# Kernel tuning notes

Measured on AMD Instinct MI355X. Metric: run time of the kernel, lower is better.

## Reference

```python
import jax, jax.numpy as jnp
import numpy as np
from itertools import product

B, C, N = 2, 64, 30000
D, H, W = 64, 64, 64


def _make_shift():
    # itertools.product over (-1,0,1)^3, scaled by 2/(size-1) per axis in (x->W, y->H, z->D) order
    s = np.array(list(product((-1, 0, 1), repeat=3)), dtype=np.float32)  # [27,3]
    scale = np.array([2.0 / (W - 1), 2.0 / (H - 1), 2.0 / (D - 1)], dtype=np.float32)
    return jnp.asarray(s * scale)  # [27,3]


def setup_inputs() -> dict:
    key = jax.random.key(0)
    k1, k2, k3 = jax.random.split(key, 3)
    voxel_features = jax.random.normal(k1, (B, C, D, H, W), dtype=jnp.float32)
    vertices = jax.random.uniform(k2, (B, N, 3), dtype=jnp.float32, minval=-1.0, maxval=1.0)
    # kaiming_normal for relu on a (C, C, 1, 27) conv kernel: std = sqrt(2 / fan_in)
    conv_w = jax.random.normal(k3, (C, C, 27), dtype=jnp.float32) * np.float32(np.sqrt(2.0 / (C * 27)))
    conv_b = jnp.zeros((C,), dtype=jnp.float32)
    return {"voxel_features": voxel_features, "vertices": vertices, "conv_w": conv_w, "conv_b": conv_b}


def _trilinear_sample(vol, grid):
    # vol: [C, D, H, W]; grid: [M, 3] normalized (x, y, z) in [-1, 1]
    # F.grid_sample semantics: mode='bilinear' (trilinear), padding_mode='border', align_corners=True
    sizes_f = jnp.array([W - 1, H - 1, D - 1], dtype=vol.dtype)
    coord = (grid + 1.0) * 0.5 * sizes_f  # unnormalize, align_corners=True
    coord = jnp.clip(coord, 0.0, sizes_f)  # border padding
    c0f = jnp.floor(coord)
    f = coord - c0f  # fractional weights [M,3]
    c0 = c0f.astype(jnp.int32)
    c1 = jnp.minimum(c0 + 1, jnp.array([W - 1, H - 1, D - 1], dtype=jnp.int32))
    x0, y0, z0 = c0[:, 0], c0[:, 1], c0[:, 2]
    x1, y1, z1 = c1[:, 0], c1[:, 1], c1[:, 2]
    fx, fy, fz = f[:, 0], f[:, 1], f[:, 2]

    def g(zi, yi, xi):
        return vol[:, zi, yi, xi]  # [C, M]

    out = (g(z0, y0, x0) * ((1 - fx) * (1 - fy) * (1 - fz))
           + g(z0, y0, x1) * (fx * (1 - fy) * (1 - fz))
           + g(z0, y1, x0) * ((1 - fx) * fy * (1 - fz))
           + g(z0, y1, x1) * (fx * fy * (1 - fz))
           + g(z1, y0, x0) * ((1 - fx) * (1 - fy) * fz)
           + g(z1, y0, x1) * (fx * (1 - fy) * fz)
           + g(z1, y1, x0) * ((1 - fx) * fy * fz)
           + g(z1, y1, x1) * (fx * fy * fz))
    return out  # [C, M]


def reference(voxel_features, vertices, conv_w, conv_b):
    shift = _make_shift()  # [27,3]
    # neighbourhood grid: [B, N, 27, 3] -> flatten to [B, N*27, 3]
    grid = (vertices[:, :, None, :] + shift[None, None, :, :]).reshape(B, N * 27, 3)
    feats = jax.vmap(_trilinear_sample)(voxel_features, grid)  # [B, C, N*27]
    feats = feats.reshape(B, C, N, 27)
    # Conv2d(C, C, kernel=(1,27)) == learned weighted sum over 27 neighbors + channel mix
    out = jnp.einsum("bcnk,ock->bno", feats, conv_w) + conv_b[None, None, :]  # [B, N, C]
    return out
```

## Files before the change

kernel.cpp:

```cpp
#include <hip/hip_runtime.h>
#include <stdint.h>

#define NBATCH 2
#define NVERT  30000
#define VOLCH  16777216ull
#define KDIM   1728
#define ASTR   (KDIM + 8)

typedef __attribute__((ext_vector_type(8))) __bf16 bf16x8;
typedef __attribute__((ext_vector_type(4))) float f32x4;

__device__ __forceinline__ float b2f(unsigned short u) {
  unsigned int x = ((unsigned int)u) << 16;
  return __builtin_bit_cast(float, x);
}

__device__ __forceinline__ unsigned short f2b(float f) {
  unsigned int u = __builtin_bit_cast(unsigned int, f);
  u = (u + 0x7FFFu + ((u >> 16) & 1u)) >> 16;
  return (unsigned short)u;
}

__global__ __launch_bounds__(256) void transpose_vox(
    const float* __restrict__ vox, unsigned short* __restrict__ T) {
  __shared__ float tile[64][65];
  const int b = blockIdx.y;
  const int zy = blockIdx.x;
  const size_t src0 = (size_t)b * 64 * 262144 + (size_t)zy * 64;
#pragma unroll
  for (int i = 0; i < 16; ++i) {
    int idx = i * 256 + threadIdx.x;
    int c = idx >> 6, x = idx & 63;
    tile[c][x] = vox[src0 + (size_t)c * 262144 + x];
  }
  __syncthreads();
  const size_t dst0 = ((size_t)b * 4096 + zy) * 4096;
#pragma unroll
  for (int i = 0; i < 16; ++i) {
    int idx = i * 256 + threadIdx.x;
    int x = idx >> 6, c = idx & 63;
    T[dst0 + x * 64 + c] = f2b(tile[c][x]);
  }
}

__global__ __launch_bounds__(256) void prep_w(
    const float* __restrict__ w, unsigned short* __restrict__ W3) {
  int t = blockIdx.x * 256 + threadIdx.x;
  int o = t / 1728;
  int rem = t - o * 1728;
  int c = rem / 27;
  int k = rem - c * 27;
  int K = k * 64 + c;
  W3[((size_t)(K >> 3) * 64 + o) * 8 + (K & 7)] = f2b(w[t]);
}

__device__ __forceinline__ void axis_setup(float v, int idx[4], float gw[3][4]) {
  float coord = (v + 1.0f) * 0.5f * 63.0f;
  coord = fminf(fmaxf(coord, 0.0f), 63.0f);
  int b0 = (int)coord;
  if (b0 > 63) b0 = 63;
#pragma unroll
  for (int p = 0; p < 4; ++p) {
    int q = b0 - 1 + p;
    idx[p] = min(max(q, 0), 63);
  }
#pragma unroll
  for (int d = 0; d < 3; ++d) {
    float t = coord + (float)(d - 1);
    float tc = fminf(fmaxf(t, 0.0f), 63.0f);
    float fl = floorf(tc);
    int i0 = (int)fl;
    if (i0 > 63) i0 = 63;
    float f = tc - fl;
    int i1 = min(i0 + 1, 63);
    int p0 = i0 - b0 + 1;
    int p1 = i1 - b0 + 1;
#pragma unroll
    for (int p = 0; p < 4; ++p) {
      float g = (p == p0) ? (1.0f - f) : 0.0f;
      g += (p == p1) ? f : 0.0f;
      gw[d][p] = g;
    }
  }
}

__global__ __launch_bounds__(256, 2) void fused_main(
    const float* __restrict__ verts, const unsigned short* __restrict__ T,
    const unsigned short* __restrict__ W3, const float* __restrict__ bias,
    float* __restrict__ out) {
  __shared__ __align__(16) unsigned short A_lds[16][ASTR];
  const int tid = threadIdx.x;
  const int wave = tid >> 6;
  const int lane = tid & 63;
  const int batch = blockIdx.y;
  const int n0 = blockIdx.x * 16;

  const unsigned short* Tb = T + (size_t)batch * VOLCH + lane;

#pragma unroll 1
  for (int vl = 0; vl < 4; ++vl) {
    const int m = wave * 4 + vl;
    const size_t vbase = ((size_t)batch * NVERT + (n0 + m)) * 3;
    const float vx = verts[vbase + 0];
    const float vy = verts[vbase + 1];
    const float vz = verts[vbase + 2];

    int xi[4], yi[4], zi[4];
    float gwx[3][4], gwy[3][4], gwz[3][4];
    axis_setup(vx, xi, gwx);
    axis_setup(vy, yi, gwy);
    axis_setup(vz, zi, gwz);

    int xo[4];
#pragma unroll
    for (int p = 0; p < 4; ++p) xo[p] = xi[p] << 6;

    float fe[3][3][3];
#pragma unroll
    for (int a = 0; a < 3; ++a)
#pragma unroll
      for (int bb = 0; bb < 3; ++bb)
#pragma unroll
        for (int cc = 0; cc < 3; ++cc) fe[a][bb][cc] = 0.0f;

#pragma unroll
    for (int pz = 0; pz < 4; ++pz) {
      float ryv[3][3];
#pragma unroll
      for (int a = 0; a < 3; ++a)
#pragma unroll
        for (int bb = 0; bb < 3; ++bb) ryv[a][bb] = 0.0f;
      const int zoff = zi[pz] << 18;
#pragma unroll
      for (int py = 0; py < 4; ++py) {
        const unsigned short* rp = Tb + zoff + (yi[py] << 12);
        float v0 = b2f(rp[xo[0]]);
        float v1 = b2f(rp[xo[1]]);
        float v2 = b2f(rp[xo[2]]);
        float v3 = b2f(rp[xo[3]]);
        const float wy0 = gwy[0][py], wy1 = gwy[1][py], wy2 = gwy[2][py];
#pragma unroll
        for (int dx = 0; dx < 3; ++dx) {
          float rx = v0 * gwx[dx][0] + v1 * gwx[dx][1] +
                     v2 * gwx[dx][2] + v3 * gwx[dx][3];
          ryv[0][dx] += rx * wy0;
          ryv[1][dx] += rx * wy1;
          ryv[2][dx] += rx * wy2;
        }
      }
#pragma unroll
      for (int dz = 0; dz < 3; ++dz) {
        const float wz = gwz[dz][pz];
#pragma unroll
        for (int dy = 0; dy < 3; ++dy)
#pragma unroll
          for (int dx = 0; dx < 3; ++dx) fe[dz][dy][dx] += ryv[dy][dx] * wz;
      }
    }

    unsigned short* arow = &A_lds[m][0];
#pragma unroll
    for (int dz = 0; dz < 3; ++dz)
#pragma unroll
      for (int dy = 0; dy < 3; ++dy)
#pragma unroll
        for (int dx = 0; dx < 3; ++dx) {
          int k = dx * 9 + dy * 3 + dz;
          arow[(k << 6) + lane] = f2b(fe[dz][dy][dx]);
        }
  }
  __syncthreads();

  const int g = lane >> 4;
  const int r = lane & 15;
  const int o0 = wave * 16;
  f32x4 acc = {0.0f, 0.0f, 0.0f, 0.0f};
  const unsigned short* aptr = &A_lds[r][g * 8];
  const unsigned short* bptr = W3 + (size_t)(g * 64 + o0 + r) * 8;
  for (int kk = 0; kk < 54; ++kk) {
    bf16x8 a = *reinterpret_cast<const bf16x8*>(aptr + kk * 32);
    bf16x8 b = *reinterpret_cast<const bf16x8*>(bptr + (size_t)kk * 2048);
    acc = __builtin_amdgcn_mfma_f32_16x16x32_bf16(a, b, acc, 0, 0, 0);
  }

  const int oc = o0 + r;
  const float bo = bias[oc];
  float* op = out + ((size_t)batch * NVERT + n0) * 64 + oc;
#pragma unroll
  for (int i = 0; i < 4; ++i) {
    op[(size_t)(g * 4 + i) * 64] = acc[i] + bo;
  }
}

extern "C" void kernel_launch(void* const* d_in, const int* in_sizes, int n_in,
                              void* d_out, int out_size, void* d_ws, size_t ws_size,
                              hipStream_t stream) {
  const float* vox   = (const float*)d_in[0];
  const float* verts = (const float*)d_in[1];
  const float* convw = (const float*)d_in[2];
  const float* convb = (const float*)d_in[3];
  float* out = (float*)d_out;

  const size_t t_elems = (size_t)NBATCH * VOLCH;
  const size_t need = t_elems * 2 + (size_t)110592 * 2;
  if (ws_size < need) {
    hipMemsetAsync(d_out, 0xFF, (size_t)out_size * 4, stream);
    return;
  }
  unsigned short* T  = (unsigned short*)d_ws;
  unsigned short* W3 = T + t_elems;

  transpose_vox<<<dim3(4096, NBATCH), 256, 0, stream>>>(vox, T);
  prep_w<<<432, 256, 0, stream>>>(convw, W3);
  fused_main<<<dim3(NVERT / 16, NBATCH), 256, 0, stream>>>(verts, T, W3, convb, out);
}
```

Baseline: 429.1 us.

## Vectorize voxel transpose and pipeline gathers via async global-to-LDS loads

```diff
diff --git a/kernel.cpp b/kernel.cpp
--- a/kernel.cpp
+++ b/kernel.cpp
@@ -21,25 +21,45 @@
   return (unsigned short)u;
 }
 
+__device__ __forceinline__ void gload_lds16(const unsigned short* g,
+                                            unsigned short* l) {
+  __builtin_amdgcn_global_load_lds(
+      (const __attribute__((address_space(1))) void*)g,
+      (__attribute__((address_space(3))) void*)l, 16, 0, 0);
+}
+
 __global__ __launch_bounds__(256) void transpose_vox(
     const float* __restrict__ vox, unsigned short* __restrict__ T) {
-  __shared__ float tile[64][65];
+  __shared__ unsigned short tile[4][65][66];
   const int b = blockIdx.y;
-  const int zy = blockIdx.x;
-  const size_t src0 = (size_t)b * 64 * 262144 + (size_t)zy * 64;
+  const int zy0 = blockIdx.x * 4;
+  const int t = threadIdx.x;
+  const size_t src0 = (size_t)b * 64 * 262144 + (size_t)zy0 * 64;
 #pragma unroll
   for (int i = 0; i < 16; ++i) {
-    int idx = i * 256 + threadIdx.x;
-    int c = idx >> 6, x = idx & 63;
-    tile[c][x] = vox[src0 + (size_t)c * 262144 + x];
+    const int idx = i * 256 + t;
+    const int c = idx >> 6;
+    const int rem = idx & 63;
+    const int zyq = rem >> 4;
+    const int x4 = (rem & 15) << 2;
+    const float4 v = *reinterpret_cast<const float4*>(
+        vox + src0 + (size_t)c * 262144 + zyq * 64 + x4);
+    tile[zyq][c][x4 + 0] = f2b(v.x); tile[zyq][c][x4 + 1] = f2b(v.y);
+    tile[zyq][c][x4 + 2] = f2b(v.z); tile[zyq][c][x4 + 3] = f2b(v.w);
   }
   __syncthreads();
-  const size_t dst0 = ((size_t)b * 4096 + zy) * 4096;
+  const size_t dst0 = ((size_t)b * 4096 + zy0) * 4096;
 #pragma unroll
   for (int i = 0; i < 16; ++i) {
-    int idx = i * 256 + threadIdx.x;
-    int x = idx >> 6, c = idx & 63;
-    T[dst0 + x * 64 + c] = f2b(tile[c][x]);
+    const int idx = i * 256 + t;
+    const int c4 = (idx & 15) << 2;
+    const int pr = idx >> 4;
+    const int zyq = pr >> 6;
+    const int x = pr & 63;
+    ushort4 o;
+    o.x = tile[zyq][c4 + 0][x]; o.y = tile[zyq][c4 + 1][x];
+    o.z = tile[zyq][c4 + 2][x]; o.w = tile[zyq][c4 + 3][x];
+    *reinterpret_cast<ushort4*>(T + dst0 + ((size_t)zyq * 64 + x) * 64 + c4) = o;
   }
 }
 
@@ -54,23 +74,42 @@
   W3[((size_t)(K >> 3) * 64 + o) * 8 + (K & 7)] = f2b(w[t]);
 }
 
-__device__ __forceinline__ void axis_setup(float v, int idx[4], float gw[3][4]) {
-  float coord = (v + 1.0f) * 0.5f * 63.0f;
-  coord = fminf(fmaxf(coord, 0.0f), 63.0f);
+struct Idx3 {
+  int x0, x1, x2, x3;
+  int y0, y1, y2, y3;
+  int z0, z1, z2, z3;
+};
+
+__device__ __forceinline__ int clamp63(int q) { return min(max(q, 0), 63); }
+
+__device__ __forceinline__ int axis_b0(float v) {
+  float coord = fminf(fmaxf((v + 1.0f) * 0.5f * 63.0f, 0.0f), 63.0f);
   int b0 = (int)coord;
-  if (b0 > 63) b0 = 63;
-#pragma unroll
-  for (int p = 0; p < 4; ++p) {
-    int q = b0 - 1 + p;
-    idx[p] = min(max(q, 0), 63);
-  }
+  return min(b0, 63);
+}
+
+__device__ __forceinline__ Idx3 make_idx(float vx, float vy, float vz) {
+  Idx3 I;
+  int bx = axis_b0(vx), by = axis_b0(vy), bz = axis_b0(vz);
+  I.x0 = clamp63(bx - 1) << 6;  I.x1 = clamp63(bx) << 6;
+  I.x2 = clamp63(bx + 1) << 6;  I.x3 = clamp63(bx + 2) << 6;
+  I.y0 = clamp63(by - 1) << 12; I.y1 = clamp63(by) << 12;
+  I.y2 = clamp63(by + 1) << 12; I.y3 = clamp63(by + 2) << 12;
+  I.z0 = clamp63(bz - 1) << 18; I.z1 = clamp63(bz) << 18;
+  I.z2 = clamp63(bz + 1) << 18; I.z3 = clamp63(bz + 2) << 18;
+  return I;
+}
+
+struct W12 { float x[3][4], y[3][4], z[3][4]; };
+
+__device__ __forceinline__ void axis_w(float v, float gw[3][4]) {
+  float coord = fminf(fmaxf((v + 1.0f) * 0.5f * 63.0f, 0.0f), 63.0f);
+  int b0 = min((int)coord, 63);
 #pragma unroll
   for (int d = 0; d < 3; ++d) {
-    float t = coord + (float)(d - 1);
-    float tc = fminf(fmaxf(t, 0.0f), 63.0f);
+    float tc = fminf(fmaxf(coord + (float)(d - 1), 0.0f), 63.0f);
     float fl = floorf(tc);
-    int i0 = (int)fl;
-    if (i0 > 63) i0 = 63;
+    int i0 = min((int)fl, 63);
     float f = tc - fl;
     int i1 = min(i0 + 1, 63);
     int p0 = i0 - b0 + 1;
@@ -84,81 +123,116 @@
   }
 }
 
-__global__ __launch_bounds__(256, 2) void fused_main(
+__device__ __forceinline__ W12 make_w(float vx, float vy, float vz) {
+  W12 W;
+  axis_w(vx, W.x); axis_w(vy, W.y); axis_w(vz, W.z);
+  return W;
+}
+
+__device__ __forceinline__ void issue_half(
+    const unsigned short* Tbase, int zA, int zB, int y_even, int y_odd,
+    int xo_lane, unsigned short* rawX) {
+  gload_lds16(Tbase + zA + y_even + xo_lane, rawX + 0 * 512);
+  gload_lds16(Tbase + zA + y_odd  + xo_lane, rawX + 1 * 512);
+  gload_lds16(Tbase + zB + y_even + xo_lane, rawX + 2 * 512);
+  gload_lds16(Tbase + zB + y_odd  + xo_lane, rawX + 3 * 512);
+}
+
+template <int H>
+__device__ __forceinline__ void fold_half(
+    const unsigned short* rawX, const W12& W, float fe[3][3][3], int lane) {
+#pragma unroll
+  for (int pzh = 0; pzh < 2; ++pzh) {
+    const int pz = 2 * H + pzh;
+    float ry[3][3];
+#pragma unroll
+    for (int a = 0; a < 3; ++a)
+#pragma unroll
+      for (int b = 0; b < 3; ++b) ry[a][b] = 0.0f;
+#pragma unroll
+    for (int py = 0; py < 4; ++py) {
+      const unsigned short* rp = rawX + ((pzh * 16 + py * 4) << 6) + lane;
+      float v0 = b2f(rp[0]);
+      float v1 = b2f(rp[64]);
+      float v2 = b2f(rp[128]);
+      float v3 = b2f(rp[192]);
+      const float wy0 = W.y[0][py], wy1 = W.y[1][py], wy2 = W.y[2][py];
+#pragma unroll
+      for (int dx = 0; dx < 3; ++dx) {
+        float rx = v0 * W.x[dx][0] + v1 * W.x[dx][1] +
+                   v2 * W.x[dx][2] + v3 * W.x[dx][3];
+        ry[0][dx] += rx * wy0;
+        ry[1][dx] += rx * wy1;
+        ry[2][dx] += rx * wy2;
+      }
+    }
+#pragma unroll
+    for (int dz = 0; dz < 3; ++dz) {
+      const float wz = W.z[dz][pz];
+#pragma unroll
+      for (int dy = 0; dy < 3; ++dy)
+#pragma unroll
+        for (int dx = 0; dx < 3; ++dx) fe[dz][dy][dx] += ry[dy][dx] * wz;
+    }
+  }
+}
+
+__global__ __launch_bounds__(256) void fused_main(
     const float* __restrict__ verts, const unsigned short* __restrict__ T,
     const unsigned short* __restrict__ W3, const float* __restrict__ bias,
     float* __restrict__ out) {
-  __shared__ __align__(16) unsigned short A_lds[16][ASTR];
+  __shared__ __align__(16) unsigned short A_lds[8][ASTR];
+  __shared__ __align__(16) unsigned short raw[4][2][2048];
   const int tid = threadIdx.x;
   const int wave = tid >> 6;
   const int lane = tid & 63;
   const int batch = blockIdx.y;
-  const int n0 = blockIdx.x * 16;
-
-  const unsigned short* Tb = T + (size_t)batch * VOLCH + lane;
-
-#pragma unroll 1
-  for (int vl = 0; vl < 4; ++vl) {
-    const int m = wave * 4 + vl;
-    const size_t vbase = ((size_t)batch * NVERT + (n0 + m)) * 3;
-    const float vx = verts[vbase + 0];
-    const float vy = verts[vbase + 1];
-    const float vz = verts[vbase + 2];
-
-    int xi[4], yi[4], zi[4];
-    float gwx[3][4], gwy[3][4], gwz[3][4];
-    axis_setup(vx, xi, gwx);
-    axis_setup(vy, yi, gwy);
-    axis_setup(vz, zi, gwz);
-
-    int xo[4];
-#pragma unroll
-    for (int p = 0; p < 4; ++p) xo[p] = xi[p] << 6;
-
-    float fe[3][3][3];
-#pragma unroll
-    for (int a = 0; a < 3; ++a)
-#pragma unroll
-      for (int bb = 0; bb < 3; ++bb)
-#pragma unroll
-        for (int cc = 0; cc < 3; ++cc) fe[a][bb][cc] = 0.0f;
-
-#pragma unroll
-    for (int pz = 0; pz < 4; ++pz) {
-      float ryv[3][3];
-#pragma unroll
-      for (int a = 0; a < 3; ++a)
-#pragma unroll
-        for (int bb = 0; bb < 3; ++bb) ryv[a][bb] = 0.0f;
-      const int zoff = zi[pz] << 18;
-#pragma unroll
-      for (int py = 0; py < 4; ++py) {
-        const unsigned short* rp = Tb + zoff + (yi[py] << 12);
-        float v0 = b2f(rp[xo[0]]);
-        float v1 = b2f(rp[xo[1]]);
-        float v2 = b2f(rp[xo[2]]);
-        float v3 = b2f(rp[xo[3]]);
-        const float wy0 = gwy[0][py], wy1 = gwy[1][py], wy2 = gwy[2][py];
-#pragma unroll
-        for (int dx = 0; dx < 3; ++dx) {
-          float rx = v0 * gwx[dx][0] + v1 * gwx[dx][1] +
-                     v2 * gwx[dx][2] + v3 * gwx[dx][3];
-          ryv[0][dx] += rx * wy0;
-          ryv[1][dx] += rx * wy1;
-          ryv[2][dx] += rx * wy2;
-        }
-      }
-#pragma unroll
-      for (int dz = 0; dz < 3; ++dz) {
-        const float wz = gwz[dz][pz];
-#pragma unroll
-        for (int dy = 0; dy < 3; ++dy)
-#pragma unroll
-          for (int dx = 0; dx < 3; ++dx) fe[dz][dy][dx] += ryv[dy][dx] * wz;
-      }
-    }
-
-    unsigned short* arow = &A_lds[m][0];
+  const int n0 = blockIdx.x * 8;
+
+  const unsigned short* Tbase = T + (size_t)batch * VOLCH;
+  unsigned short* rawA = &raw[wave][0][0];
+  unsigned short* rawB = &raw[wave][1][0];
+  const int m0 = wave * 2;
+
+  const size_t vb = ((size_t)batch * NVERT + (n0 + m0)) * 3;
+  const float ax = verts[vb + 0], ay = verts[vb + 1], az = verts[vb + 2];
+  const float bx = verts[vb + 3], by = verts[vb + 4], bz = verts[vb + 5];
+
+  const int ce = (lane & 7) << 3;
+  const int px = (lane >> 3) & 3;
+
+  const Idx3 IA = make_idx(ax, ay, az);
+  const int xoA = (px & 2 ? (px & 1 ? IA.x3 : IA.x2)
+                          : (px & 1 ? IA.x1 : IA.x0)) + ce;
+  const int yeA = (lane & 32) ? IA.y1 : IA.y0;
+  const int yoA = (lane & 32) ? IA.y3 : IA.y2;
+  issue_half(Tbase, IA.z0, IA.z1, yeA, yoA, xoA, rawA);
+  issue_half(Tbase, IA.z2, IA.z3, yeA, yoA, xoA, rawB);
+
+  const W12 WA = make_w(ax, ay, az);
+  const Idx3 IB = make_idx(bx, by, bz);
+  const int xoB = (px & 2 ? (px & 1 ? IB.x3 : IB.x2)
+                          : (px & 1 ? IB.x1 : IB.x0)) + ce;
+  const int yeB = (lane & 32) ? IB.y1 : IB.y0;
+  const int yoB = (lane & 32) ? IB.y3 : IB.y2;
+
+  float fe[3][3][3];
+#pragma unroll
+  for (int a = 0; a < 3; ++a)
+#pragma unroll
+    for (int b = 0; b < 3; ++b)
+#pragma unroll
+      for (int c = 0; c < 3; ++c) fe[a][b][c] = 0.0f;
+
+  asm volatile("s_waitcnt vmcnt(4)" ::: "memory");
+  fold_half<0>(rawA, WA, fe, lane);
+  issue_half(Tbase, IB.z0, IB.z1, yeB, yoB, xoB, rawA);
+  asm volatile("s_waitcnt vmcnt(4)" ::: "memory");
+  fold_half<1>(rawB, WA, fe, lane);
+  issue_half(Tbase, IB.z2, IB.z3, yeB, yoB, xoB, rawB);
+
+  {
+    unsigned short* arow = &A_lds[m0][0];
 #pragma unroll
     for (int dz = 0; dz < 3; ++dz)
 #pragma unroll
@@ -169,14 +243,41 @@
           arow[(k << 6) + lane] = f2b(fe[dz][dy][dx]);
         }
   }
+
+  const W12 WB = make_w(bx, by, bz);
+  float fe2[3][3][3];
+#pragma unroll
+  for (int a = 0; a < 3; ++a)
+#pragma unroll
+    for (int b = 0; b < 3; ++b)
+#pragma unroll
+      for (int c = 0; c < 3; ++c) fe2[a][b][c] = 0.0f;
+
+  asm volatile("s_waitcnt vmcnt(4)" ::: "memory");
+  fold_half<0>(rawA, WB, fe2, lane);
+  asm volatile("s_waitcnt vmcnt(0)" ::: "memory");
+  fold_half<1>(rawB, WB, fe2, lane);
+  {
+    unsigned short* arow = &A_lds[m0 + 1][0];
+#pragma unroll
+    for (int dz = 0; dz < 3; ++dz)
+#pragma unroll
+      for (int dy = 0; dy < 3; ++dy)
+#pragma unroll
+        for (int dx = 0; dx < 3; ++dx) {
+          int k = dx * 9 + dy * 3 + dz;
+          arow[(k << 6) + lane] = f2b(fe2[dz][dy][dx]);
+        }
+  }
   __syncthreads();
 
   const int g = lane >> 4;
   const int r = lane & 15;
   const int o0 = wave * 16;
   f32x4 acc = {0.0f, 0.0f, 0.0f, 0.0f};
-  const unsigned short* aptr = &A_lds[r][g * 8];
+  const unsigned short* aptr = &A_lds[r & 7][g * 8];
   const unsigned short* bptr = W3 + (size_t)(g * 64 + o0 + r) * 8;
+#pragma unroll 1
   for (int kk = 0; kk < 54; ++kk) {
     bf16x8 a = *reinterpret_cast<const bf16x8*>(aptr + kk * 32);
     bf16x8 b = *reinterpret_cast<const bf16x8*>(bptr + (size_t)kk * 2048);
@@ -185,10 +286,12 @@
 
   const int oc = o0 + r;
   const float bo = bias[oc];
-  float* op = out + ((size_t)batch * NVERT + n0) * 64 + oc;
-#pragma unroll
-  for (int i = 0; i < 4; ++i) {
-    op[(size_t)(g * 4 + i) * 64] = acc[i] + bo;
+  if (g < 2) {
+    float* op = out + ((size_t)batch * NVERT + n0) * 64 + oc;
+#pragma unroll
+    for (int i = 0; i < 4; ++i) {
+      op[(size_t)(g * 4 + i) * 64] = acc[i] + bo;
+    }
   }
 }
 
@@ -210,7 +313,7 @@
   unsigned short* T  = (unsigned short*)d_ws;
   unsigned short* W3 = T + t_elems;
 
-  transpose_vox<<<dim3(4096, NBATCH), 256, 0, stream>>>(vox, T);
+  transpose_vox<<<dim3(1024, NBATCH), 256, 0, stream>>>(vox, T);
   prep_w<<<432, 256, 0, stream>>>(convw, W3);
-  fused_main<<<dim3(NVERT / 16, NBATCH), 256, 0, stream>>>(verts, T, W3, convb, out);
-}
+  fused_main<<<dim3(NVERT / 8, NBATCH), 256, 0, stream>>>(verts, T, W3, convb, out);
+}
```

Result: slower. 486.4 us (+13.4%).
